# Performance work log

Hardware: AMD Instinct MI355X
Metric: run time of the kernel (lower is better)

## Reference

```python
import jax, jax.numpy as jnp
import numpy as np

MAX_SET_SIZE = 32  # f1_query_max_set_size


def setup_inputs() -> dict:
    key = jax.random.key(0)
    k1, k2, k3, k4 = jax.random.split(key, 4)
    B, Lq, L, d_qk, d_v = 8, 512, 4096, 64, 64
    q = jax.random.normal(k1, (B, Lq, d_qk), dtype=jnp.float32)
    k = jax.random.normal(k2, (B, L, d_qk), dtype=jnp.float32)
    v = jax.random.normal(k3, (B, L, d_v), dtype=jnp.float32)
    mask = jax.random.randint(k4, (B * Lq, L), 0, 2).astype(bool)
    return {"q": q, "k": k, "v": v, "mask": mask}


def _query_conditioned_subset_pool(rank_scores, v, batch_idx, mask, max_set_size):
    # rank_scores/mask: [N, L]; v: [B, L, d_v]
    N, L = rank_scores.shape
    keep = min(max_set_size, L)
    neg_inf = jnp.finfo(rank_scores.dtype).min
    masked_scores = jnp.where(mask, rank_scores.astype(jnp.float32), neg_inf)
    _, top_idx = jax.lax.top_k(masked_scores, keep)          # [N, keep]
    picked = jnp.take_along_axis(mask, top_idx, axis=1)
    sortable = jnp.where(picked, top_idx, L)                 # sentinel L for unpicked
    sortable = jnp.sort(sortable, axis=1)                    # restore index order
    picked = sortable < L
    safe_idx = jnp.where(picked, sortable, 0)                # [N, keep]
    sel_v = v[batch_idx[:, None], safe_idx]                  # [N, keep, d_v]
    sel_scores = jnp.take_along_axis(rank_scores, safe_idx, axis=1)
    sel_scores = jnp.where(picked, sel_scores, neg_inf)
    attn = jax.nn.softmax(sel_scores, axis=1)
    non_empty = picked.any(axis=1, keepdims=True)
    attn = jnp.where(picked & non_empty, attn, jnp.zeros_like(attn))
    return jnp.einsum('nk,nkd->nd', attn.astype(sel_v.dtype), sel_v)


def reference(q, k, v, mask):
    B, Lq, d_qk = q.shape
    L = k.shape[1]
    d_v = v.shape[-1]
    scale = 1.0 / float(np.sqrt(d_qk))
    # rank_scores [B, Lq, L] -> flat chains [B*Lq, L]
    rank_scores = jnp.einsum('bqd,bld->bql', q, k) * scale
    rs_flat = rank_scores.reshape(B * Lq, L)
    batch_idx = jnp.repeat(jnp.arange(B), Lq)
    # f1 = mean over masked support: sum_v / clamp(count, 1)
    mask_f = mask.astype(q.dtype)                            # [B*Lq, L]
    count = jnp.clip(mask_f.sum(axis=1), 1.0, None)          # [B*Lq]
    sum_v = jnp.einsum('bql,bld->bqd', mask_f.reshape(B, Lq, L), v).reshape(B * Lq, d_v)
    mean_out = sum_v / count[:, None]
    # f1_query_mode='add': query-conditioned restricted pooling over top-k subset
    q_ctx = _query_conditioned_subset_pool(rs_flat, v, batch_idx, mask, MAX_SET_SIZE)
    out = mean_out + q_ctx
    return out.reshape(B, Lq, d_v)
```

## Files before the change

### kernel.cpp

```cpp
#include <hip/hip_runtime.h>
#include <float.h>
#include <math.h>

#define LQ   512
#define LL   4096
#define DD   64
#define KEEP 32
#define NB   8
#define NROWS (NB * LQ)

#define RT    32
#define NLC   8
#define LC    (LL / NLC)
#define LSP   128
#define NPAIR (LC / LSP)

#define WS_VT    (NROWS * LL)
#define WS_PC    (WS_VT + (NB * DD * LL) / 2)
#define WS_TOTAL (WS_PC + 4 * NROWS)

#define MASKED_KEY 0x00800000u

typedef short  bf16x8 __attribute__((ext_vector_type(8)));
typedef float  f32x4  __attribute__((ext_vector_type(4)));

__device__ __forceinline__ float dot4(float4 a, float4 b) {
    return a.x * b.x + a.y * b.y + a.z * b.z + a.w * b.w;
}
__device__ __forceinline__ unsigned short f2bf(float f) {
    unsigned int u = __float_as_uint(f);
    return (unsigned short)((u + 0x7FFFu + ((u >> 16) & 1u)) >> 16);
}

#define TP_LB 256
__global__ __launch_bounds__(256) void k_vt(
    const float* __restrict__ v, unsigned short* __restrict__ vt)
{
    __shared__ unsigned short tile[DD][TP_LB + 8];
    const int t  = threadIdx.x;
    const int b  = blockIdx.x >> 4;
    const int l0 = (blockIdx.x & 15) * TP_LB;

    const float4* vg = reinterpret_cast<const float4*>(v + ((size_t)b * LL + l0) * DD);
    #pragma unroll
    for (int i = 0; i < 16; ++i) {
        int j = t + 256 * i;
        float4 f = vg[j];
        int l = j >> 4, dq = (j & 15) * 4;
        tile[dq + 0][l] = f2bf(f.x);
        tile[dq + 1][l] = f2bf(f.y);
        tile[dq + 2][l] = f2bf(f.z);
        tile[dq + 3][l] = f2bf(f.w);
    }
    __syncthreads();
    const int d = t >> 2, seg = t & 3;
    const uint4* src = reinterpret_cast<const uint4*>(&tile[d][seg * 64]);
    uint4* dst = reinterpret_cast<uint4*>(vt + ((size_t)b * DD + d) * LL + l0 + seg * 64);
    #pragma unroll
    for (int i = 0; i < 8; ++i) dst[i] = src[i];
}

__global__ __launch_bounds__(256) void k_mean(
    const int* __restrict__ mask,
    const unsigned short* __restrict__ vt,
    float* __restrict__ out,
    float* __restrict__ pcnt)
{
    __shared__ float sums[4][4][16][16];
    __shared__ float cnt_s[4][16];

    const int t     = threadIdx.x;
    const int wave  = t >> 6;
    const int lane  = t & 63;
    const int lcq   = blockIdx.x & 3;
    const int rg    = blockIdx.x >> 2;
    const int n0    = rg * 16;
    const int b     = n0 / LQ;
    const int row_a = lane & 15;
    const int chunk = lane >> 4;
    const int lb    = lcq * 1024 + wave * 256;

    const int* mrow = mask + (size_t)(n0 + row_a) * LL + lb + chunk * 8;
    const unsigned short* vbase = vt + (size_t)b * DD * LL + lb + chunk * 8;

    f32x4 acc[4];
    #pragma unroll
    for (int dt = 0; dt < 4; ++dt) acc[dt] = (f32x4){0.f, 0.f, 0.f, 0.f};
    int cnt = 0;

    for (int l0 = 0; l0 < 256; l0 += 32) {
        int4 ma = *reinterpret_cast<const int4*>(mrow + l0);
        int4 mb = *reinterpret_cast<const int4*>(mrow + l0 + 4);
        cnt += (ma.x != 0) + (ma.y != 0) + (ma.z != 0) + (ma.w != 0)
             + (mb.x != 0) + (mb.y != 0) + (mb.z != 0) + (mb.w != 0);
        unsigned int p[4];
        p[0] = (ma.x ? 0x3F80u : 0u) | (ma.y ? 0x3F800000u : 0u);
        p[1] = (ma.z ? 0x3F80u : 0u) | (ma.w ? 0x3F800000u : 0u);
        p[2] = (mb.x ? 0x3F80u : 0u) | (mb.y ? 0x3F800000u : 0u);
        p[3] = (mb.z ? 0x3F80u : 0u) | (mb.w ? 0x3F800000u : 0u);
        bf16x8 afrag = *reinterpret_cast<bf16x8*>(p);
        #pragma unroll
        for (int dt = 0; dt < 4; ++dt) {
            bf16x8 bfrag = *reinterpret_cast<const bf16x8*>(
                vbase + (size_t)(dt * 16 + row_a) * LL + l0);
            acc[dt] = __builtin_amdgcn_mfma_f32_16x16x32_bf16(afrag, bfrag, acc[dt], 0, 0, 0);
        }
    }
    cnt += __shfl_xor(cnt, 16);
    cnt += __shfl_xor(cnt, 32);
    if (lane < 16) cnt_s[wave][lane] = (float)cnt;
    #pragma unroll
    for (int dt = 0; dt < 4; ++dt)
        #pragma unroll
        for (int r = 0; r < 4; ++r)
            sums[wave][dt][chunk * 4 + r][row_a] = acc[dt][r];
    __syncthreads();

    const int d = t & 63, rgrp = t >> 6;
    #pragma unroll
    for (int rr = 0; rr < 4; ++rr) {
        const int row = rgrp * 4 + rr;
        float s = sums[0][d >> 4][row][d & 15] + sums[1][d >> 4][row][d & 15]
                + sums[2][d >> 4][row][d & 15] + sums[3][d >> 4][row][d & 15];
        float c = cnt_s[0][row] + cnt_s[1][row] + cnt_s[2][row] + cnt_s[3][row];
        atomicAdd(&out[(size_t)(n0 + row) * DD + d], s);
        if (d == 0) pcnt[lcq * NROWS + n0 + row] = c;
    }
}

__global__ __launch_bounds__(256)
__attribute__((amdgpu_waves_per_eu(2, 4)))
void k_scores(
    const float* __restrict__ q,
    const float* __restrict__ kmat,
    const int*   __restrict__ mask,
    float*       __restrict__ ws_sc)
{
    __shared__ float4 Ss4[16 * LSP];

    const int t    = threadIdx.x;
    const int wave = t >> 6;
    const int lane = t & 63;
    const int rt   = blockIdx.x >> 3;
    const int lc   = blockIdx.x & (NLC - 1);
    const int n0   = rt * RT;
    const int b    = n0 / LQ;
    const int lbase = lc * LC;

    int qbase[8];
    #pragma unroll
    for (int p = 0; p < 8; ++p)
        qbase[p] = __builtin_amdgcn_readfirstlane((n0 + wave * 8 + p) * DD);

    const float4* kg = reinterpret_cast<const float4*>(kmat) + (size_t)b * LL * 16;

    for (int s = 0; s < NPAIR; ++s) {
        const int l0 = lbase + s * LSP;
        __syncthreads();
        #pragma unroll
        for (int i = 0; i < 2; ++i)
            #pragma unroll
            for (int j = 0; j < 4; ++j)
                Ss4[(wave * 4 + j) * LSP + lane + 64 * i] =
                    kg[(size_t)(l0 + lane + 64 * i) * 16 + wave * 4 + j];
        __syncthreads();

        float acc0[8], acc1[8];
        #pragma unroll
        for (int p = 0; p < 8; ++p) { acc0[p] = 0.f; acc1[p] = 0.f; }
        #pragma unroll
        for (int dc = 0; dc < 16; ++dc) {
            float4 ka = Ss4[dc * LSP + lane];
            float4 kb = Ss4[dc * LSP + 64 + lane];
            #pragma unroll
            for (int p = 0; p < 8; ++p) {
                float4 q4 = *reinterpret_cast<const float4*>(q + qbase[p] + dc * 4);
                acc0[p] += dot4(ka, q4);
                acc1[p] += dot4(kb, q4);
            }
        }
        #pragma unroll
        for (int p = 0; p < 8; ++p) {
            const int r = wave * 8 + p;
            int m0 = mask[(size_t)(n0 + r) * LL + l0 + lane];
            int m1 = mask[(size_t)(n0 + r) * LL + l0 + 64 + lane];
            ws_sc[(size_t)(n0 + r) * LL + l0 + lane]      = m0 ? acc0[p] * 0.125f : -FLT_MAX;
            ws_sc[(size_t)(n0 + r) * LL + l0 + 64 + lane] = m1 ? acc1[p] * 0.125f : -FLT_MAX;
        }
    }
}

__global__ __launch_bounds__(256, 3) void k_select(
    const float* __restrict__ vmat,
    const float* __restrict__ ws,
    const float* __restrict__ pcnt,
    float*       __restrict__ out)
{
    __shared__ unsigned int hist[4][256];
    __shared__ unsigned int selKey[4][KEEP];
    __shared__ int          selIdx[4][KEEP];
    __shared__ float        wsel[4][KEEP];
    __shared__ int          selCnt[4], eqCnt[4];

    const int t    = threadIdx.x;
    const int wave = t >> 6;
    const int lane = t & 63;
    const int row  = blockIdx.x * 4 + wave;
    const int b    = row / LQ;

    float o = out[(size_t)row * DD + lane];
    {
        float cc = pcnt[row] + pcnt[NROWS + row]
                 + pcnt[2 * NROWS + row] + pcnt[3 * NROWS + row];
        if (cc < 1.f) cc = 1.f;
        o /= cc;
    }

    unsigned int key[64];
    {
        const float4* sg = reinterpret_cast<const float4*>(ws) + (size_t)row * (LL / 4);
        #pragma unroll
        for (int i = 0; i < 16; ++i) {
            float4 f = sg[lane + 64 * i];
            float vals[4] = { f.x, f.y, f.z, f.w };
            #pragma unroll
            for (int c = 0; c < 4; ++c) {
                unsigned int u = __float_as_uint(vals[c]);
                key[4 * i + c] = ((int)u < 0) ? ~u : (u | 0x80000000u);
            }
        }
    }

    unsigned int prefix = 0, quota = KEEP;
    #pragma unroll
    for (int pass = 0; pass < 4; ++pass) {
        const int shift = 24 - 8 * pass;
        const unsigned int hs = (pass == 0) ? 0u : (unsigned int)(32 - 8 * pass);
        reinterpret_cast<uint4*>(hist[wave])[lane] = make_uint4(0u, 0u, 0u, 0u);
        __asm__ volatile("s_waitcnt lgkmcnt(0)" ::: "memory");
        #pragma unroll
        for (int e = 0; e < 64; ++e) {
            bool act = (pass == 0) || ((key[e] >> hs) == prefix);
            if (act) atomicAdd(&hist[wave][(key[e] >> shift) & 255u], 1u);
        }
        __asm__ volatile("s_waitcnt lgkmcnt(0)" ::: "memory");
        uint4 h = reinterpret_cast<const uint4*>(hist[wave])[lane];
        unsigned int s4  = h.x + h.y + h.z + h.w;
        unsigned int suf = s4;
        #pragma unroll
        for (int off = 1; off < 64; off <<= 1) {
            unsigned int v = (unsigned int)__shfl_down((int)suf, off);
            if (lane + off < 64) suf += v;
        }
        unsigned int above = suf - s4;
        bool cond = (suf >= quota) && (above < quota);
        unsigned int Bq = 0, nq = 0;
        if (cond) {
            unsigned int hb[4] = { h.x, h.y, h.z, h.w };
            unsigned int run = above;
            int Bj = 0;
            #pragma unroll
            for (int j = 3; j >= 0; --j) {
                unsigned int nb = run + hb[j];
                if (nb >= quota) { Bj = j; break; }
                run = nb;
            }
            Bq = (unsigned int)(lane * 4 + Bj);
            nq = quota - run;
        }
        unsigned long long bal = __ballot(cond);
        int src = __ffsll(bal) - 1;
        Bq = (unsigned int)__shfl((int)Bq, src);
        nq = (unsigned int)__shfl((int)nq, src);
        prefix = (prefix << 8) | Bq;
        quota  = nq;
    }
    const unsigned int T = prefix;
    const bool take_eq = (T != MASKED_KEY);

    if (lane < KEEP) { wsel[wave][lane] = 0.f; selIdx[wave][lane] = 0; }
    if (lane == 0)   { selCnt[wave] = 0; eqCnt[wave] = 0; }
    __asm__ volatile("s_waitcnt lgkmcnt(0)" ::: "memory");
    #pragma unroll
    for (int e = 0; e < 64; ++e) {
        unsigned int k = key[e];
        if (k > T) {
            int slot = atomicAdd(&selCnt[wave], 1);
            selKey[wave][slot] = k;
            selIdx[wave][slot] = 256 * (e >> 2) + 4 * lane + (e & 3);
        } else if (take_eq && k == T) {
            int t2 = atomicAdd(&eqCnt[wave], 1);
            if (t2 < (int)quota) {
                int slot = atomicAdd(&selCnt[wave], 1);
                selKey[wave][slot] = k;
                selIdx[wave][slot] = 256 * (e >> 2) + 4 * lane + (e & 3);
            }
        }
    }
    __asm__ volatile("s_waitcnt lgkmcnt(0)" ::: "memory");
    const int S = selCnt[wave];

    if (S > 0) {
        float vj = -FLT_MAX;
        if (lane < S) {
            unsigned int kk = selKey[wave][lane];
            unsigned int u = (kk & 0x80000000u) ? (kk ^ 0x80000000u) : ~kk;
            vj = __uint_as_float(u);
        }
        float mx = vj;
        #pragma unroll
        for (int off = 1; off < 64; off <<= 1) mx = fmaxf(mx, __shfl_xor(mx, off));
        float e = (lane < S) ? expf(vj - mx) : 0.f;
        float sum = e;
        #pragma unroll
        for (int off = 1; off < 64; off <<= 1) sum += __shfl_xor(sum, off);
        if (lane < S) wsel[wave][lane] = e / sum;
        __asm__ volatile("s_waitcnt lgkmcnt(0)" ::: "memory");
        const float* vb = vmat + (size_t)b * LL * DD + lane;
        #pragma unroll
        for (int j = 0; j < KEEP; ++j) {
            float wj = wsel[wave][j];
            int   ij = selIdx[wave][j];
            o += wj * vb[(size_t)ij * DD];
        }
    }
    out[(size_t)row * DD + lane] = o;
}

#define QT   2
#define NT   256
#define NTILES (LL / NT)

__global__ __launch_bounds__(NT, 4) void ga_fused_fb(
    const float* __restrict__ q, const float* __restrict__ kmat,
    const float* __restrict__ vmat, const int* __restrict__ mask,
    float* __restrict__ out)
{
    __shared__ float sc[QT][LL];
    __shared__ float q_s[QT][DD];
    __shared__ unsigned long long mbits[QT][LL / 64];
    __shared__ float redv[4][QT][DD];
    __shared__ float mean_s[QT][DD];
    __shared__ int   count_s[QT];
    __shared__ int   sel_idx[QT][KEEP];
    __shared__ float sel_val[QT][KEEP];
    __shared__ int   sel_cnt[QT];
    __shared__ float wred[4];
    __shared__ int   ired[4];
    __shared__ int   brk;
    __shared__ float wgt[QT][KEEP];

    const int t = threadIdx.x, wave = t >> 6, lane = t & 63;
    const int n0 = blockIdx.x * QT, b = n0 / LQ;

    if (t < QT) sel_cnt[t] = 0;
    if (t < QT * DD) q_s[t >> 6][t & 63] = q[(size_t)(n0 + (t >> 6)) * DD + (t & 63)];
    __syncthreads();

    const float4* q4_0 = reinterpret_cast<const float4*>(&q_s[0][0]);
    const float4* q4_1 = reinterpret_cast<const float4*>(&q_s[1][0]);
    for (int tile = 0; tile < NTILES; ++tile) {
        int l = tile * NT + t;
        const float4* kr = reinterpret_cast<const float4*>(kmat + (size_t)(b * LL + l) * DD);
        float d0 = 0.f, d1 = 0.f;
        #pragma unroll
        for (int i = 0; i < 16; ++i) {
            float4 kk = kr[i], qa = q4_0[i], qb = q4_1[i];
            d0 += kk.x * qa.x + kk.y * qa.y + kk.z * qa.z + kk.w * qa.w;
            d1 += kk.x * qb.x + kk.y * qb.y + kk.z * qb.z + kk.w * qb.w;
        }
        int mv0 = mask[(size_t)n0 * LL + l];
        int mv1 = mask[(size_t)(n0 + 1) * LL + l];
        unsigned long long b0 = __ballot(mv0 != 0);
        unsigned long long b1 = __ballot(mv1 != 0);
        if (lane == 0) { mbits[0][tile * 4 + wave] = b0; mbits[1][tile * 4 + wave] = b1; }
        sc[0][l] = mv0 ? d0 * 0.125f : -FLT_MAX;
        sc[1][l] = mv1 ? d1 * 0.125f : -FLT_MAX;
    }
    __syncthreads();

    if (wave < QT) {
        int c = (int)__popcll(mbits[wave][lane]);
        for (int off = 32; off >= 1; off >>= 1) c += __shfl_down(c, off);
        if (lane == 0) count_s[wave] = c;
    }
    {
        float acc0 = 0.f, acc1 = 0.f;
        const int g = wave, d = lane;
        for (int wi = 0; wi < LL / 64; ++wi) {
            unsigned long long w0 = mbits[0][wi], w1 = mbits[1][wi];
            const float* vp = vmat + (size_t)(b * LL + wi * 64 + g) * DD + d;
            #pragma unroll 4
            for (int ii = 0; ii < 16; ++ii) {
                int sh = g + 4 * ii;
                float vv = vp[(size_t)(4 * ii) * DD];
                if ((w0 >> sh) & 1ULL) acc0 += vv;
                if ((w1 >> sh) & 1ULL) acc1 += vv;
            }
        }
        redv[g][0][d] = acc0; redv[g][1][d] = acc1;
    }
    __syncthreads();
    if (t < QT * DD) {
        int qt = t >> 6, dd = t & 63;
        float s2 = redv[0][qt][dd] + redv[1][qt][dd] + redv[2][qt][dd] + redv[3][qt][dd];
        int c = count_s[qt]; if (c < 1) c = 1;
        mean_s[qt][dd] = s2 / (float)c;
    }
    __syncthreads();

    for (int qt = 0; qt < QT; ++qt) {
        for (int s = 0; s < KEEP; ++s) {
            float m = -FLT_MAX; int mi = LL;
            for (int j = 0; j < NTILES; ++j) {
                int l = j * NT + t;
                float val = sc[qt][l];
                if (val > m) { m = val; mi = l; }
            }
            for (int off = 32; off >= 1; off >>= 1) {
                float ov = __shfl_down(m, off);
                int   oi = __shfl_down(mi, off);
                if (ov > m || (ov == m && oi < mi)) { m = ov; mi = oi; }
            }
            if (lane == 0) { wred[wave] = m; ired[wave] = mi; }
            __syncthreads();
            if (t == 0) {
                float bv = wred[0]; int bi = ired[0];
                for (int w2 = 1; w2 < 4; ++w2) {
                    float ov = wred[w2]; int oi = ired[w2];
                    if (ov > bv || (ov == bv && oi < bi)) { bv = ov; bi = oi; }
                }
                if (bv > -FLT_MAX) {
                    sel_idx[qt][s] = bi; sel_val[qt][s] = bv; sel_cnt[qt] = s + 1;
                    sc[qt][bi] = -FLT_MAX; brk = 0;
                } else brk = 1;
            }
            __syncthreads();
            if (brk) break;
        }
    }

    if (wave < QT) {
        int qt = wave, S = sel_cnt[qt];
        if (S > 0) {
            float mx = sel_val[qt][0];
            float e = 0.f;
            if (lane < S) e = expf(sel_val[qt][lane] - mx);
            float ssum = e;
            for (int off = 32; off >= 1; off >>= 1) ssum += __shfl_xor(ssum, off);
            if (lane < S) wgt[qt][lane] = e / ssum;
        }
    }
    __syncthreads();
    if (wave < QT) {
        int qt = wave, S = sel_cnt[qt];
        float o = mean_s[qt][lane];
        for (int j = 0; j < S; ++j)
            o += wgt[qt][j] * vmat[(size_t)(b * LL + sel_idx[qt][j]) * DD + lane];
        out[(size_t)(n0 + qt) * DD + lane] = o;
    }
}

extern "C" void kernel_launch(void* const* d_in, const int* in_sizes, int n_in,
                              void* d_out, int out_size, void* d_ws, size_t ws_size,
                              hipStream_t stream) {
    const float* q    = (const float*)d_in[0];
    const float* kmat = (const float*)d_in[1];
    const float* vmat = (const float*)d_in[2];
    const int*   mask = (const int*)d_in[3];
    float* out = (float*)d_out;

    const size_t need = (size_t)WS_TOTAL * sizeof(float);
    if (ws_size >= need) {
        float* ws = (float*)d_ws;
        unsigned short* vt = (unsigned short*)(ws + WS_VT);
        float* pcnt = ws + WS_PC;
        hipMemsetAsync(out, 0, (size_t)NROWS * DD * sizeof(float), stream);
        hipLaunchKernelGGL(k_scores, dim3((NROWS / RT) * NLC), dim3(256), 0, stream,
                           q, kmat, mask, ws);
        hipLaunchKernelGGL(k_vt, dim3(NB * 16), dim3(256), 0, stream, vmat, vt);
        hipLaunchKernelGGL(k_mean, dim3((NROWS / 16) * 4), dim3(256), 0, stream,
                           mask, vt, out, pcnt);
        hipLaunchKernelGGL(k_select, dim3(NROWS / 4), dim3(256), 0, stream,
                           vmat, ws, pcnt, out);
    } else {
        hipLaunchKernelGGL(ga_fused_fb, dim3(NROWS / QT), dim3(NT), 0, stream,
                           q, kmat, vmat, mask, out);
    }
}
```

Before: 293.7 us.

## Restructure score kernel to hold key row in registers per thread

```diff
diff --git a/kernel.cpp b/kernel.cpp
--- a/kernel.cpp
+++ b/kernel.cpp
@@ -8,12 +8,6 @@
 #define KEEP 32
 #define NB   8
 #define NROWS (NB * LQ)
-
-#define RT    32
-#define NLC   8
-#define LC    (LL / NLC)
-#define LSP   128
-#define NPAIR (LC / LSP)
 
 #define WS_VT    (NROWS * LL)
 #define WS_PC    (WS_VT + (NB * DD * LL) / 2)
@@ -128,65 +122,46 @@
     }
 }
 
-__global__ __launch_bounds__(256)
-__attribute__((amdgpu_waves_per_eu(2, 4)))
-void k_scores(
+__global__ __launch_bounds__(256) void k_scores(
     const float* __restrict__ q,
     const float* __restrict__ kmat,
     const int*   __restrict__ mask,
     float*       __restrict__ ws_sc)
 {
-    __shared__ float4 Ss4[16 * LSP];
-
     const int t    = threadIdx.x;
     const int wave = t >> 6;
     const int lane = t & 63;
-    const int rt   = blockIdx.x >> 3;
-    const int lc   = blockIdx.x & (NLC - 1);
-    const int n0   = rt * RT;
+    const int lc   = blockIdx.x & 15;
+    const int rg   = blockIdx.x >> 4;
+    const int n0   = rg * 16;
     const int b    = n0 / LQ;
-    const int lbase = lc * LC;
-
-    int qbase[8];
-    #pragma unroll
-    for (int p = 0; p < 8; ++p)
-        qbase[p] = __builtin_amdgcn_readfirstlane((n0 + wave * 8 + p) * DD);
-
-    const float4* kg = reinterpret_cast<const float4*>(kmat) + (size_t)b * LL * 16;
-
-    for (int s = 0; s < NPAIR; ++s) {
-        const int l0 = lbase + s * LSP;
-        __syncthreads();
-        #pragma unroll
-        for (int i = 0; i < 2; ++i)
-            #pragma unroll
-            for (int j = 0; j < 4; ++j)
-                Ss4[(wave * 4 + j) * LSP + lane + 64 * i] =
-                    kg[(size_t)(l0 + lane + 64 * i) * 16 + wave * 4 + j];
-        __syncthreads();
-
-        float acc0[8], acc1[8];
-        #pragma unroll
-        for (int p = 0; p < 8; ++p) { acc0[p] = 0.f; acc1[p] = 0.f; }
-        #pragma unroll
-        for (int dc = 0; dc < 16; ++dc) {
-            float4 ka = Ss4[dc * LSP + lane];
-            float4 kb = Ss4[dc * LSP + 64 + lane];
-            #pragma unroll
-            for (int p = 0; p < 8; ++p) {
-                float4 q4 = *reinterpret_cast<const float4*>(q + qbase[p] + dc * 4);
-                acc0[p] += dot4(ka, q4);
-                acc1[p] += dot4(kb, q4);
-            }
-        }
-        #pragma unroll
-        for (int p = 0; p < 8; ++p) {
-            const int r = wave * 8 + p;
-            int m0 = mask[(size_t)(n0 + r) * LL + l0 + lane];
-            int m1 = mask[(size_t)(n0 + r) * LL + l0 + 64 + lane];
-            ws_sc[(size_t)(n0 + r) * LL + l0 + lane]      = m0 ? acc0[p] * 0.125f : -FLT_MAX;
-            ws_sc[(size_t)(n0 + r) * LL + l0 + 64 + lane] = m1 ? acc1[p] * 0.125f : -FLT_MAX;
-        }
+    const int l    = lc * 256 + wave * 64 + lane;
+
+    const float4* kr = reinterpret_cast<const float4*>(kmat + ((size_t)b * LL + l) * DD);
+    float4 kreg[16];
+    #pragma unroll
+    for (int i = 0; i < 16; ++i) kreg[i] = kr[i];
+
+    int mreg[16];
+    #pragma unroll
+    for (int p = 0; p < 16; ++p)
+        mreg[p] = mask[(size_t)(n0 + p) * LL + l];
+
+    const int qb = __builtin_amdgcn_readfirstlane(n0 * DD);
+    #pragma unroll
+    for (int p = 0; p < 16; ++p) {
+        const float4* qp = reinterpret_cast<const float4*>(q + qb + p * DD);
+        float ax = 0.f, ay = 0.f, az = 0.f, aw = 0.f;
+        #pragma unroll
+        for (int i = 0; i < 16; ++i) {
+            float4 qv = qp[i];
+            ax = fmaf(qv.x, kreg[i].x, ax);
+            ay = fmaf(qv.y, kreg[i].y, ay);
+            az = fmaf(qv.z, kreg[i].z, az);
+            aw = fmaf(qv.w, kreg[i].w, aw);
+        }
+        float acc = ax + ay + az + aw;
+        ws_sc[(size_t)(n0 + p) * LL + l] = mreg[p] ? acc * 0.125f : -FLT_MAX;
     }
 }
 
@@ -476,7 +451,7 @@
         unsigned short* vt = (unsigned short*)(ws + WS_VT);
         float* pcnt = ws + WS_PC;
         hipMemsetAsync(out, 0, (size_t)NROWS * DD * sizeof(float), stream);
-        hipLaunchKernelGGL(k_scores, dim3((NROWS / RT) * NLC), dim3(256), 0, stream,
+        hipLaunchKernelGGL(k_scores, dim3(4096), dim3(256), 0, stream,
                            q, kmat, mask, ws);
         hipLaunchKernelGGL(k_vt, dim3(NB * 16), dim3(256), 0, stream, vmat, vt);
         hipLaunchKernelGGL(k_mean, dim3((NROWS / 16) * 4), dim3(256), 0, stream,
```

New measurement: 253.7 us. -13.6%, faster.
